# Kernel optimization log

Hardware: AMD Instinct MI355X
Metric: run time of the kernel (lower is better)

Reference implementation:

```python
import jax, jax.numpy as jnp
import numpy as np

B, N, D, E, H, HS = 2, 1024, 256, 64, 8, 64
FF = 4 * D
EPS = 1e-6


def _glorot(key, shape):
    fan_in, fan_out = shape[-2], shape[-1]
    lim = np.sqrt(6.0 / (fan_in + fan_out))
    return jax.random.uniform(key, shape, jnp.float32, -lim, lim)


def setup_inputs() -> dict:
    key = jax.random.key(0)
    ks = jax.random.split(key, 10)
    return {
        "node": jax.random.normal(ks[0], (B, N, D), jnp.float32),
        "edge": jax.random.normal(ks[1], (B, N, N, E), jnp.float32),
        "Wq": _glorot(ks[2], (H, D, HS)),
        "Wk": _glorot(ks[3], (H, D + E, HS)),
        "Wv": _glorot(ks[4], (H, D, HS)),
        "Wp": _glorot(ks[5], (H, HS, D)),
        "bp": jnp.zeros((D,), jnp.float32),
        "ln1_g": jnp.ones((D,), jnp.float32),
        "ln1_b": jnp.zeros((D,), jnp.float32),
        "W1": _glorot(ks[6], (D, FF)),
        "b1": jnp.zeros((FF,), jnp.float32),
        "W2": _glorot(ks[7], (FF, D)),
        "b2": jnp.zeros((D,), jnp.float32),
        "ln2_g": jnp.ones((D,), jnp.float32),
        "ln2_b": jnp.zeros((D,), jnp.float32),
    }


def _layernorm(x, g, b):
    mu = jnp.mean(x, axis=-1, keepdims=True)
    var = jnp.mean(jnp.square(x - mu), axis=-1, keepdims=True)
    return (x - mu) * jax.lax.rsqrt(var + EPS) * g + b


def reference(node, edge, Wq, Wk, Wv, Wp, bp, ln1_g, ln1_b, W1, b1, W2, b2, ln2_g, ln2_b):
    d_in = node.shape[-1]
    head_size = Wq.shape[-1]
    # query projection, scaled by sqrt(head_size)
    q = jnp.einsum('bni,hio->bnho', node, Wq) / jnp.sqrt(jnp.asarray(head_size, node.dtype))
    # key kernel split: node part [H, D, HS] and edge part [H, E, HS].
    # concat([repeat(key), edge]) @ Wk  ==  key @ Wk[:, :D] + edge @ Wk[:, D:]
    kn = jnp.einsum('bmi,hio->bmho', node, Wk[:, :d_in])          # [B,M,H,HS]
    logits = jnp.einsum('bnho,bmho->bhnm', q, kn)                 # node-key logits
    qe = jnp.einsum('bnho,heo->bnhe', q, Wk[:, d_in:])            # [B,N,H,E]
    logits = logits + jnp.einsum('bnhe,bnme->bhnm', qe, edge)     # edge-conditioned logits
    attn = jax.nn.softmax(logits, axis=-1)                        # [B,H,N,M]
    v = jnp.einsum('bmi,hio->bmho', node, Wv)                     # [B,M,H,HS]
    mo = jnp.einsum('bhnm,bmho->bnho', attn, v)                   # [B,N,H,HS]
    mha = jnp.einsum('bnhi,hio->bno', mo, Wp) + bp                # output projection
    # residual + layernorm (dropout = identity at eval)
    x = _layernorm(node + mha, ln1_g, ln1_b)
    # FFN: one hidden layer of ff_multi*D with relu, then project back to D
    ff = jax.nn.relu(x @ W1 + b1) @ W2 + b2
    return _layernorm(x + ff, ln2_g, ln2_b)
```

## Files before the change

kernel.cpp:

```cpp
#include <hip/hip_runtime.h>
#include <hip/hip_bf16.h>
#include <hip/hip_fp16.h>

#define B_  2
#define N_  1024
#define D_  256
#define E_  64
#define H_  8
#define HS_ 64
#define FF_ 1024
#define R_  (B_*N_)

typedef short bf8 __attribute__((ext_vector_type(8)));
typedef float f4  __attribute__((ext_vector_type(4)));

static __device__ __forceinline__ ushort f2b(float f) {
  __hip_bfloat16 h = __float2bfloat16(f);
  return *reinterpret_cast<ushort*>(&h);
}

static __device__ __forceinline__ ushort4 f4_to_b4(float4 v) {
  ushort4 r;
  r.x = f2b(v.x); r.y = f2b(v.y); r.z = f2b(v.z); r.w = f2b(v.w);
  return r;
}

__global__ void k_pack(const float* __restrict__ node, const float* __restrict__ Wq,
                       const float* __restrict__ Wk, const float* __restrict__ Wv,
                       const float* __restrict__ Wp, const float* __restrict__ W1,
                       const float* __restrict__ W2,
                       ushort* __restrict__ node_bf, ushort* __restrict__ wqkvT,
                       ushort* __restrict__ wkeT, ushort* __restrict__ wpT,
                       ushort* __restrict__ w1T, ushort* __restrict__ w2T) {
  int idx = blockIdx.x * 256 + threadIdx.x;
  if (idx < 524288) {
    node_bf[idx] = f2b(node[idx]);
    return;
  }
  idx -= 524288;
  if (idx < 393216) {
    int c = idx >> 8, i = idx & 255;
    int mat = c >> 9, h = (c >> 6) & 7, o = c & 63;
    float v;
    if (mat == 0)      v = Wq[(h * 256 + i) * 64 + o] * 0.125f;
    else if (mat == 1) v = Wk[(h * 320 + i) * 64 + o];
    else               v = Wv[(h * 256 + i) * 64 + o];
    wqkvT[idx] = f2b(v);
    return;
  }
  idx -= 393216;
  if (idx < 262144) {
    int c = idx >> 9, r = idx & 511;
    int h2 = c >> 6, e = c & 63, h = r >> 6, o = r & 63;
    wkeT[idx] = (h2 == h) ? f2b(Wk[(h * 320 + 256 + e) * 64 + o]) : (ushort)0;
    return;
  }
  idx -= 262144;
  if (idx < 131072) {
    int c = idx >> 9, r = idx & 511;
    wpT[idx] = f2b(Wp[r * 256 + c]);
    return;
  }
  idx -= 131072;
  if (idx < 262144) {
    int c = idx >> 8, k = idx & 255;
    w1T[idx] = f2b(W1[k * 1024 + c]);
    return;
  }
  idx -= 262144;
  {
    int c = idx >> 10, k = idx & 1023;
    w2T[idx] = f2b(W2[k * 256 + c]);
  }
}

__global__ void k_vT(const ushort* __restrict__ qkv, ushort* __restrict__ vt) {
  int idx = blockIdx.x * 256 + threadIdx.x;
  if (idx >= 16 * 64 * 1024) return;
  int m = idx & 1023;
  int rest = idx >> 10;
  int o = rest & 63;
  int bh = rest >> 6;
  int b = bh >> 3, h = bh & 7;
  vt[idx] = qkv[(size_t)(b * 1024 + m) * 1536 + 1024 + h * 64 + o];
}

template<int EPI, int OFMT, int NBT, bool BDIAG>
__global__ void k_gemm(const ushort* __restrict__ A, const ushort* __restrict__ Bt,
                       void* __restrict__ Cv, const float* __restrict__ bias,
                       int M, int N, int K, int lda, int ldbt, int ldc,
                       long long as1, long long as2, long long bs1, long long bs2,
                       long long cs1, long long cs2) {
  int z = blockIdx.z;
  const ushort* Ab = A  + (size_t)((z >> 3) * as1 + (z & 7) * as2);
  const ushort* Bb = Bt + (size_t)((z >> 3) * bs1 + (z & 7) * bs2);
  size_t coff = (size_t)((z >> 3) * cs1 + (z & 7) * cs2);
  int r0 = blockIdx.x * 64, c0 = blockIdx.y * (64 * NBT);

  __shared__ ushort As[64][40];
  __shared__ ushort Bs[64 * NBT][40];

  int tid = threadIdx.x;
  int lane = tid & 63, w = tid >> 6;
  int wm = w >> 1, wn = w & 1;
  int kg = lane >> 4, lr = lane & 15;

  f4 acc[2][2 * NBT] = {};

  int kbeg = BDIAG ? c0 : 0;
  int kend = BDIAG ? c0 + 64 : K;
  for (int k0 = kbeg; k0 < kend; k0 += 32) {
    __syncthreads();
    {
      int row = tid >> 2, ch = tid & 3;
      *(int4*)&As[row][ch * 8] = *(const int4*)(Ab + (size_t)(r0 + row) * lda + k0 + ch * 8);
    }
    #pragma unroll
    for (int i = 0; i < NBT; ++i) {
      int row = (tid >> 2) + 64 * i, ch = tid & 3;
      *(int4*)&Bs[row][ch * 8] = *(const int4*)(Bb + (size_t)(c0 + row) * ldbt + k0 + ch * 8);
    }
    __syncthreads();

    bf8 bfr[2 * NBT];
    #pragma unroll
    for (int nt = 0; nt < NBT; ++nt)
      #pragma unroll
      for (int cb = 0; cb < 2; ++cb)
        bfr[nt * 2 + cb] = *(const bf8*)&Bs[nt * 64 + wn * 32 + cb * 16 + lr][kg * 8];
    #pragma unroll
    for (int rb = 0; rb < 2; ++rb) {
      bf8 af = *(const bf8*)&As[wm * 32 + rb * 16 + lr][kg * 8];
      #pragma unroll
      for (int q = 0; q < 2 * NBT; ++q)
        acc[rb][q] = __builtin_amdgcn_mfma_f32_16x16x32_bf16(af, bfr[q], acc[rb][q], 0, 0, 0);
    }
  }

  float*  Cf = (float*)Cv;
  ushort* Cb = (ushort*)Cv;
  __half* Ch = (__half*)Cv;
  #pragma unroll
  for (int rb = 0; rb < 2; ++rb) {
    #pragma unroll
    for (int q = 0; q < 2 * NBT; ++q) {
      #pragma unroll
      for (int rr = 0; rr < 4; ++rr) {
        int row = r0 + wm * 32 + rb * 16 + kg * 4 + rr;
        int col = c0 + (q >> 1) * 64 + wn * 32 + (q & 1) * 16 + lr;
        size_t ci = coff + (size_t)row * ldc + col;
        float v = acc[rb][q][rr];
        if (EPI >= 2) v += bias[col];
        if (EPI == 3) v = fmaxf(v, 0.0f);
        if (OFMT == 1)      Cb[ci] = f2b(v);
        else if (OFMT == 2) Ch[ci] = __float2half(v);
        else                Cf[ci] = v;
      }
    }
  }
}

__global__ __launch_bounds__(256) void k_gemm_ln(
    const ushort* __restrict__ A, const ushort* __restrict__ Bt,
    const float* __restrict__ bias, const float* __restrict__ resid,
    const float* __restrict__ g, const float* __restrict__ be,
    float* __restrict__ of, ushort* __restrict__ ob, int K) {
  int r0 = blockIdx.x * 64;
  __shared__ ushort As[64][40];
  __shared__ ushort Bs[256][40];
  int tid = threadIdx.x, lane = tid & 63, w = tid >> 6;
  int kg = lane >> 4, lr = lane & 15;

  f4 acc[16] = {};
  for (int k0 = 0; k0 < K; k0 += 32) {
    __syncthreads();
    { int row = tid >> 2, ch = tid & 3;
      *(int4*)&As[row][ch * 8] = *(const int4*)(A + (size_t)(r0 + row) * K + k0 + ch * 8); }
    #pragma unroll
    for (int j = 0; j < 4; ++j) {
      int pos = tid + 256 * j, row = pos >> 2, ch = pos & 3;
      *(int4*)&Bs[row][ch * 8] = *(const int4*)(Bt + (size_t)row * K + k0 + ch * 8);
    }
    __syncthreads();
    bf8 af = *(const bf8*)&As[w * 16 + lr][kg * 8];
    #pragma unroll
    for (int fc = 0; fc < 16; ++fc) {
      bf8 bf = *(const bf8*)&Bs[fc * 16 + lr][kg * 8];
      acc[fc] = __builtin_amdgcn_mfma_f32_16x16x32_bf16(af, bf, acc[fc], 0, 0, 0);
    }
  }

  #pragma unroll
  for (int fc = 0; fc < 16; ++fc) {
    int col = fc * 16 + lr;
    #pragma unroll
    for (int rr = 0; rr < 4; ++rr) {
      int row = r0 + w * 16 + kg * 4 + rr;
      acc[fc][rr] += bias[col] + resid[(size_t)row * 256 + col];
    }
  }
  float mean[4], rstd[4];
  #pragma unroll
  for (int rr = 0; rr < 4; ++rr) {
    float s = 0.f;
    #pragma unroll
    for (int fc = 0; fc < 16; ++fc) s += acc[fc][rr];
    #pragma unroll
    for (int off = 1; off < 16; off <<= 1) s += __shfl_xor(s, off);
    mean[rr] = s * (1.0f / 256.0f);
    float q = 0.f;
    #pragma unroll
    for (int fc = 0; fc < 16; ++fc) { float d = acc[fc][rr] - mean[rr]; q += d * d; }
    #pragma unroll
    for (int off = 1; off < 16; off <<= 1) q += __shfl_xor(q, off);
    rstd[rr] = rsqrtf(q * (1.0f / 256.0f) + 1e-6f);
  }
  #pragma unroll
  for (int fc = 0; fc < 16; ++fc) {
    int col = fc * 16 + lr;
    float gg = g[col], bb = be[col];
    #pragma unroll
    for (int rr = 0; rr < 4; ++rr) {
      int row = r0 + w * 16 + kg * 4 + rr;
      float y = (acc[fc][rr] - mean[rr]) * rstd[rr] * gg + bb;
      of[(size_t)row * 256 + col] = y;
      if (ob) ob[(size_t)row * 256 + col] = f2b(y);
    }
  }
}

__global__ __launch_bounds__(256, 4) void k_fused(
    const float* __restrict__ edge, const float* __restrict__ qe,
    const __half* __restrict__ logN, ushort* __restrict__ attn) {
  int bid = blockIdx.x;
  int b = bid >> 10, n = bid & 1023;
  int t = threadIdx.x;
  int lane = t & 63, w = t >> 6;
  int kg = lane >> 4, lr = lane & 15;

  __shared__ ushort As[128 * 64];
  __shared__ __half lg[1024 * 9];
  __shared__ float red[2][4][8];

  bf8 bq[2];
  {
    const float* qrow = qe + (size_t)bid * 512 + (size_t)(lr & 7) * 64;
    #pragma unroll
    for (int kk = 0; kk < 2; ++kk) {
      float4 a  = *reinterpret_cast<const float4*>(&qrow[kk * 32 + kg * 8]);
      float4 c4 = *reinterpret_cast<const float4*>(&qrow[kk * 32 + kg * 8 + 4]);
      bq[kk][0] = (short)f2b(a.x);  bq[kk][1] = (short)f2b(a.y);
      bq[kk][2] = (short)f2b(a.z);  bq[kk][3] = (short)f2b(a.w);
      bq[kk][4] = (short)f2b(c4.x); bq[kk][5] = (short)f2b(c4.y);
      bq[kk][6] = (short)f2b(c4.z); bq[kk][7] = (short)f2b(c4.w);
    }
  }

  const float* eb = edge + (size_t)bid * 65536;

  float4 pf[8];
  #pragma unroll
  for (int u = 0; u < 8; ++u)
    pf[u] = reinterpret_cast<const float4*>(eb)[t + 256 * u];

  #pragma unroll 1
  for (int tl = 0; tl < 8; ++tl) {
    __syncthreads();
    #pragma unroll
    for (int u = 0; u < 8; ++u) {
      int g = t + 256 * u;
      int rl = g >> 4, c = t & 15;
      int slot = (c >> 1) ^ (rl & 7), half = c & 1;
      *reinterpret_cast<ushort4*>(&As[rl * 64 + slot * 8 + half * 4]) = f4_to_b4(pf[u]);
    }
    if (tl < 7) {
      const float4* src = reinterpret_cast<const float4*>(eb + (tl + 1) * 8192);
      #pragma unroll
      for (int u = 0; u < 8; ++u) pf[u] = src[t + 256 * u];
    }
    __syncthreads();

    #pragma unroll
    for (int sub = 0; sub < 2; ++sub) {
      int sr = w * 32 + sub * 16 + lr;
      f4 acc = {};
      #pragma unroll
      for (int kk = 0; kk < 2; ++kk) {
        bf8 af = *reinterpret_cast<const bf8*>(&As[sr * 64 + (((kk * 4 + kg) ^ (sr & 7)) << 3)]);
        acc = __builtin_amdgcn_mfma_f32_16x16x32_bf16(af, bq[kk], acc, 0, 0, 0);
      }
      if (lr < 8) {
        int mbase = tl * 128 + w * 32 + sub * 16 + kg * 4;
        #pragma unroll
        for (int rr = 0; rr < 4; ++rr)
          lg[(mbase + rr) * 9 + lr] = __float2half(acc[rr]);
      }
    }
  }

  ushort lNr[4][8];
  #pragma unroll
  for (int j = 0; j < 4; ++j)
    #pragma unroll
    for (int h = 0; h < 8; ++h)
      lNr[j][h] = *reinterpret_cast<const ushort*>(
          &logN[((size_t)(b * 8 + h) * 1024 + n) * 1024 + t + 256 * j]);
  __syncthreads();

  float l[4][8];
  #pragma unroll
  for (int j = 0; j < 4; ++j) {
    int m = t + 256 * j;
    #pragma unroll
    for (int h = 0; h < 8; ++h)
      l[j][h] = __half2float(lg[m * 9 + h]) +
                __half2float(*reinterpret_cast<const __half*>(&lNr[j][h]));
  }
  float mx[8], sm[8];
  #pragma unroll
  for (int h = 0; h < 8; ++h) {
    float v = fmaxf(fmaxf(l[0][h], l[1][h]), fmaxf(l[2][h], l[3][h]));
    #pragma unroll
    for (int off = 32; off; off >>= 1) v = fmaxf(v, __shfl_xor(v, off));
    if (lane == 0) red[0][w][h] = v;
  }
  __syncthreads();
  #pragma unroll
  for (int h = 0; h < 8; ++h)
    mx[h] = fmaxf(fmaxf(red[0][0][h], red[0][1][h]), fmaxf(red[0][2][h], red[0][3][h]));
  #pragma unroll
  for (int j = 0; j < 4; ++j)
    #pragma unroll
    for (int h = 0; h < 8; ++h)
      l[j][h] = __expf(l[j][h] - mx[h]);
  #pragma unroll
  for (int h = 0; h < 8; ++h) {
    float v = l[0][h] + l[1][h] + l[2][h] + l[3][h];
    #pragma unroll
    for (int off = 32; off; off >>= 1) v += __shfl_xor(v, off);
    if (lane == 0) red[1][w][h] = v;
  }
  __syncthreads();
  #pragma unroll
  for (int h = 0; h < 8; ++h)
    sm[h] = 1.0f / (red[1][0][h] + red[1][1][h] + red[1][2][h] + red[1][3][h]);
  #pragma unroll
  for (int h = 0; h < 8; ++h) {
    size_t base = ((size_t)(b * 8 + h) * 1024 + n) * 1024;
    #pragma unroll
    for (int j = 0; j < 4; ++j)
      attn[base + t + 256 * j] = f2b(l[j][h] * sm[h]);
  }
}


extern "C" void kernel_launch(void* const* d_in, const int* in_sizes, int n_in,
                              void* d_out, int out_size, void* d_ws, size_t ws_size,
                              hipStream_t stream) {
  (void)in_sizes; (void)n_in; (void)out_size; (void)ws_size;
  const float* node = (const float*)d_in[0];
  const float* edge = (const float*)d_in[1];
  const float* Wq   = (const float*)d_in[2];
  const float* Wk   = (const float*)d_in[3];
  const float* Wv   = (const float*)d_in[4];
  const float* Wp   = (const float*)d_in[5];
  const float* bp   = (const float*)d_in[6];
  const float* g1   = (const float*)d_in[7];
  const float* be1  = (const float*)d_in[8];
  const float* W1   = (const float*)d_in[9];
  const float* b1   = (const float*)d_in[10];
  const float* W2   = (const float*)d_in[11];
  const float* b2   = (const float*)d_in[12];
  const float* g2   = (const float*)d_in[13];
  const float* be2  = (const float*)d_in[14];
  float* out = (float*)d_out;

  char* ws = (char*)d_ws;
  size_t off = 0;
  auto alloc = [&](size_t bytes) -> char* {
    char* p = ws + off;
    off = (off + bytes + 255) & ~(size_t)255;
    return p;
  };
  ushort* node_bf = (ushort*)alloc((size_t)R_ * D_ * 2);
  ushort* wqkvT   = (ushort*)alloc((size_t)1536 * 256 * 2);
  ushort* wkeT    = (ushort*)alloc((size_t)512 * 512 * 2);
  ushort* wpT     = (ushort*)alloc((size_t)256 * 512 * 2);
  ushort* w1T     = (ushort*)alloc((size_t)1024 * 256 * 2);
  ushort* w2T     = (ushort*)alloc((size_t)256 * 1024 * 2);
  ushort* qkv     = (ushort*)alloc((size_t)R_ * 1536 * 2);
  float*  qe      = (float*) alloc((size_t)R_ * 512 * 4);
  ushort* vt      = (ushort*)alloc((size_t)16 * 64 * 1024 * 2);
  __half* logits  = (__half*)alloc((size_t)16 * 1024 * 1024 * 2);
  ushort* attn    = (ushort*)alloc((size_t)16 * 1024 * 1024 * 2);
  ushort* mo      = (ushort*)alloc((size_t)R_ * 512 * 2);
  float*  xf      = (float*) alloc((size_t)R_ * 256 * 4);
  ushort* xb      = (ushort*)alloc((size_t)R_ * 256 * 2);
  ushort* hb      = (ushort*)alloc((size_t)R_ * 1024 * 2);

  k_pack<<<dim3(7168), dim3(256), 0, stream>>>(node, Wq, Wk, Wv, Wp, W1, W2,
                                               node_bf, wqkvT, wkeT, wpT, w1T, w2T);

  k_gemm<0, 1, 1, false><<<dim3(32, 24, 1), dim3(256), 0, stream>>>(
      node_bf, wqkvT, qkv, nullptr, 2048, 1536, 256, 256, 256, 1536,
      0LL, 0LL, 0LL, 0LL, 0LL, 0LL);

  k_gemm<0, 0, 1, true><<<dim3(32, 8, 1), dim3(256), 0, stream>>>(
      qkv, wkeT, qe, nullptr, 2048, 512, 512, 1536, 512, 512,
      0LL, 0LL, 0LL, 0LL, 0LL, 0LL);

  k_vT<<<dim3(4096), dim3(256), 0, stream>>>(qkv, vt);

  k_gemm<0, 2, 4, false><<<dim3(16, 4, 16), dim3(256), 0, stream>>>(
      qkv, qkv + 512, logits, nullptr, 1024, 1024, 64, 1536, 1536, 1024,
      1572864LL, 64LL, 1572864LL, 64LL, 8388608LL, 1048576LL);

  k_fused<<<dim3(2048), dim3(256), 0, stream>>>(edge, qe, logits, attn);

  k_gemm<0, 1, 1, false><<<dim3(16, 1, 16), dim3(256), 0, stream>>>(
      attn, vt, mo, nullptr, 1024, 64, 1024, 1024, 1024, 512,
      8388608LL, 1048576LL, 524288LL, 65536LL, 524288LL, 64LL);

  k_gemm_ln<<<dim3(32), dim3(256), 0, stream>>>(
      mo, wpT, bp, node, g1, be1, xf, xb, 512);

  k_gemm<3, 1, 1, false><<<dim3(32, 16, 1), dim3(256), 0, stream>>>(
      xb, w1T, hb, b1, 2048, 1024, 256, 256, 256, 1024,
      0LL, 0LL, 0LL, 0LL, 0LL, 0LL);

  k_gemm_ln<<<dim3(32), dim3(256), 0, stream>>>(
      hb, w2T, b2, xf, g2, be2, out, nullptr, 1024);
}
```

Measured before the change: 250.2 us.

## Split GEMM+LayerNorm rows across more blocks with cross-wave reduction

The fused GEMM+LayerNorm kernel now handles 16 rows per block instead of 64, with each of the four waves owning a 64-column slice rather than a 16-row slice. Row mean and variance are combined across waves through a small shared-memory reduction with extra barriers. The grid grows from 32 to 128 blocks so more compute units are busy on this 2048-row problem. In exchange, each block reloads the full 256-column weight tile for fewer rows, so total weight traffic rises, and two more syncs are added.

```diff
diff --git a/kernel.cpp b/kernel.cpp
--- a/kernel.cpp
+++ b/kernel.cpp
@@ -165,63 +165,91 @@
     const float* __restrict__ bias, const float* __restrict__ resid,
     const float* __restrict__ g, const float* __restrict__ be,
     float* __restrict__ of, ushort* __restrict__ ob, int K) {
-  int r0 = blockIdx.x * 64;
-  __shared__ ushort As[64][40];
+  int r0 = blockIdx.x * 16;
+  __shared__ ushort As[16][40];
   __shared__ ushort Bs[256][40];
+  __shared__ float redL[2][4][16];
   int tid = threadIdx.x, lane = tid & 63, w = tid >> 6;
   int kg = lane >> 4, lr = lane & 15;
 
-  f4 acc[16] = {};
+  f4 acc[4] = {};
   for (int k0 = 0; k0 < K; k0 += 32) {
     __syncthreads();
-    { int row = tid >> 2, ch = tid & 3;
-      *(int4*)&As[row][ch * 8] = *(const int4*)(A + (size_t)(r0 + row) * K + k0 + ch * 8); }
+    if (tid < 64) {
+      int row = tid >> 2, ch = tid & 3;
+      *(int4*)&As[row][ch * 8] = *(const int4*)(A + (size_t)(r0 + row) * K + k0 + ch * 8);
+    }
     #pragma unroll
     for (int j = 0; j < 4; ++j) {
       int pos = tid + 256 * j, row = pos >> 2, ch = pos & 3;
       *(int4*)&Bs[row][ch * 8] = *(const int4*)(Bt + (size_t)row * K + k0 + ch * 8);
     }
     __syncthreads();
-    bf8 af = *(const bf8*)&As[w * 16 + lr][kg * 8];
-    #pragma unroll
-    for (int fc = 0; fc < 16; ++fc) {
-      bf8 bf = *(const bf8*)&Bs[fc * 16 + lr][kg * 8];
+    bf8 af = *(const bf8*)&As[lr][kg * 8];
+    #pragma unroll
+    for (int fc = 0; fc < 4; ++fc) {
+      bf8 bf = *(const bf8*)&Bs[w * 64 + fc * 16 + lr][kg * 8];
       acc[fc] = __builtin_amdgcn_mfma_f32_16x16x32_bf16(af, bf, acc[fc], 0, 0, 0);
     }
   }
 
   #pragma unroll
-  for (int fc = 0; fc < 16; ++fc) {
-    int col = fc * 16 + lr;
+  for (int fc = 0; fc < 4; ++fc) {
+    int col = w * 64 + fc * 16 + lr;
     #pragma unroll
     for (int rr = 0; rr < 4; ++rr) {
-      int row = r0 + w * 16 + kg * 4 + rr;
+      int row = r0 + kg * 4 + rr;
       acc[fc][rr] += bias[col] + resid[(size_t)row * 256 + col];
     }
   }
-  float mean[4], rstd[4];
+  float s[4];
   #pragma unroll
   for (int rr = 0; rr < 4; ++rr) {
-    float s = 0.f;
-    #pragma unroll
-    for (int fc = 0; fc < 16; ++fc) s += acc[fc][rr];
-    #pragma unroll
-    for (int off = 1; off < 16; off <<= 1) s += __shfl_xor(s, off);
-    mean[rr] = s * (1.0f / 256.0f);
-    float q = 0.f;
-    #pragma unroll
-    for (int fc = 0; fc < 16; ++fc) { float d = acc[fc][rr] - mean[rr]; q += d * d; }
-    #pragma unroll
-    for (int off = 1; off < 16; off <<= 1) q += __shfl_xor(q, off);
-    rstd[rr] = rsqrtf(q * (1.0f / 256.0f) + 1e-6f);
-  }
-  #pragma unroll
-  for (int fc = 0; fc < 16; ++fc) {
-    int col = fc * 16 + lr;
+    float v = acc[0][rr] + acc[1][rr] + acc[2][rr] + acc[3][rr];
+    #pragma unroll
+    for (int off = 1; off < 16; off <<= 1) v += __shfl_xor(v, off);
+    s[rr] = v;
+  }
+  if (lr == 0) {
+    #pragma unroll
+    for (int rr = 0; rr < 4; ++rr) redL[0][w][kg * 4 + rr] = s[rr];
+  }
+  __syncthreads();
+  float mean[4];
+  #pragma unroll
+  for (int rr = 0; rr < 4; ++rr) {
+    int row = kg * 4 + rr;
+    mean[rr] = (redL[0][0][row] + redL[0][1][row] + redL[0][2][row] + redL[0][3][row])
+               * (1.0f / 256.0f);
+  }
+  #pragma unroll
+  for (int rr = 0; rr < 4; ++rr) {
+    float v = 0.f;
+    #pragma unroll
+    for (int fc = 0; fc < 4; ++fc) { float d = acc[fc][rr] - mean[rr]; v += d * d; }
+    #pragma unroll
+    for (int off = 1; off < 16; off <<= 1) v += __shfl_xor(v, off);
+    s[rr] = v;
+  }
+  if (lr == 0) {
+    #pragma unroll
+    for (int rr = 0; rr < 4; ++rr) redL[1][w][kg * 4 + rr] = s[rr];
+  }
+  __syncthreads();
+  float rstd[4];
+  #pragma unroll
+  for (int rr = 0; rr < 4; ++rr) {
+    int row = kg * 4 + rr;
+    rstd[rr] = rsqrtf((redL[1][0][row] + redL[1][1][row] + redL[1][2][row] + redL[1][3][row])
+                      * (1.0f / 256.0f) + 1e-6f);
+  }
+  #pragma unroll
+  for (int fc = 0; fc < 4; ++fc) {
+    int col = w * 64 + fc * 16 + lr;
     float gg = g[col], bb = be[col];
     #pragma unroll
     for (int rr = 0; rr < 4; ++rr) {
-      int row = r0 + w * 16 + kg * 4 + rr;
+      int row = r0 + kg * 4 + rr;
       float y = (acc[fc][rr] - mean[rr]) * rstd[rr] * gg + bb;
       of[(size_t)row * 256 + col] = y;
       if (ob) ob[(size_t)row * 256 + col] = f2b(y);
@@ -421,13 +449,13 @@
       attn, vt, mo, nullptr, 1024, 64, 1024, 1024, 1024, 512,
       8388608LL, 1048576LL, 524288LL, 65536LL, 524288LL, 64LL);
 
-  k_gemm_ln<<<dim3(32), dim3(256), 0, stream>>>(
+  k_gemm_ln<<<dim3(128), dim3(256), 0, stream>>>(
       mo, wpT, bp, node, g1, be1, xf, xb, 512);
 
   k_gemm<3, 1, 1, false><<<dim3(32, 16, 1), dim3(256), 0, stream>>>(
       xb, w1T, hb, b1, 2048, 1024, 256, 256, 256, 1024,
       0LL, 0LL, 0LL, 0LL, 0LL, 0LL);
 
-  k_gemm_ln<<<dim3(32), dim3(256), 0, stream>>>(
+  k_gemm_ln<<<dim3(128), dim3(256), 0, stream>>>(
       hb, w2T, b2, xf, g2, be2, out, nullptr, 1024);
 }
```

Result: slower. 270.1 us (+8.0%).
